# Kernel tuning notes

Measured on AMD Instinct MI355X. Metric: run time of the kernel, lower is better.

Reference implementation:

```python
import jax, jax.numpy as jnp
import numpy as np

B, N, D, H = 256, 40, 256, 256      # molecules, atoms/molecule, pc_hidden, pred_hidden
nS, nC, nB = 40, 5, 5               # n_SYMBOLS, n_FORMAL_CHARGES, n_BOND_TYPES
NEG_SLOPE = 0.01                    # F.leaky_relu default


def _lrelu(x):
    return jnp.where(x >= 0, x, NEG_SLOPE * x)


def setup_inputs() -> dict:
    key = jax.random.key(0)
    ks = jax.random.split(key, 7)
    def w(k, shape, fan_in):
        return jax.random.normal(k, shape, jnp.float32) / np.float32(np.sqrt(fan_in))
    return {
        "yhat": jax.random.normal(ks[0], (B, N, D), jnp.float32),
        "Ws1": w(ks[1], (D, H), D),      "bs1": jnp.zeros((H,), jnp.float32),
        "Ws2": w(ks[2], (H, nS), H),     "bs2": jnp.zeros((nS,), jnp.float32),
        "Wc1": w(ks[3], (D, H), D),      "bc1": jnp.zeros((H,), jnp.float32),
        "Wc2": w(ks[4], (H, nC), H),     "bc2": jnp.zeros((nC,), jnp.float32),
        "Wb1": w(ks[5], (2 * D, H), 2 * D), "bb1": jnp.zeros((H,), jnp.float32),
        "Wb2": w(ks[6], (H, nB), H),     "bb2": jnp.zeros((nB,), jnp.float32),
    }


def reference(yhat, Ws1, bs1, Ws2, bs2, Wc1, bc1, Wc2, bc2, Wb1, bb1, Wb2, bb2):
    # Per-atom symbol / charge heads (2-layer MLP with leaky_relu)
    symbols = _lrelu(yhat @ Ws1 + bs1) @ Ws2 + bs2          # [B, N, nS]
    charges = _lrelu(yhat @ Wc1 + bc1) @ Wc2 + bc2          # [B, N, nC]

    # Pairwise bond head: concat(x_i, x_j) @ Wb1 == x_i @ Wb1[:D] + x_j @ Wb1[D:]
    # (avoids materializing the [B, N, N, 2D] concat tensor)
    p1 = yhat @ Wb1[:D]                                      # [B, N, H]
    p2 = yhat @ Wb1[D:]                                      # [B, N, H]
    h = _lrelu(p1[:, :, None, :] + p2[:, None, :, :] + bb1)  # [B, N, N, H]
    bonds = h @ Wb2 + bb2                                    # [B, N, N, nB]
    bonds = bonds + jnp.swapaxes(bonds, 1, 2)                # symmetrize (i,j)+(j,i)

    return (symbols.reshape(-1, nS),
            charges.reshape(-1, nC),
            bonds.reshape(-1, nB))
```

## Files before the change

kernel.cpp:

```cpp
#include <hip/hip_runtime.h>
#include <hip/hip_bf16.h>

typedef unsigned short u16;
typedef __attribute__((ext_vector_type(4))) int   int4v;
typedef __attribute__((ext_vector_type(4))) unsigned int uint4v;
typedef __attribute__((ext_vector_type(4))) unsigned short ushort4v;
typedef __attribute__((ext_vector_type(4))) float floatx4;
typedef __attribute__((ext_vector_type(8))) short bf16x8;
typedef _Float16 half8 __attribute__((ext_vector_type(8)));
typedef _Float16 half2v __attribute__((ext_vector_type(2)));

#define LRELU_NS 0.01f
#define SK 264

__device__ __forceinline__ float bitsToF(unsigned int b) {
    union { unsigned int u; float f; } v; v.u = b << 16; return v.f;
}
__device__ __forceinline__ u16 f2bf(float f) {
    __hip_bfloat16 h = __float2bfloat16(f);
    return *reinterpret_cast<u16*>(&h);
}
__device__ __forceinline__ float lrelu(float v) {
    return fmaxf(v, LRELU_NS * v);
}
__device__ __forceinline__ u16 ldW(const void* p, int i, int isF32) {
    return isF32 ? f2bf(((const float*)p)[i]) : ((const u16*)p)[i];
}
__device__ __forceinline__ float ldF(const void* p, int i, int isF32) {
    return isF32 ? ((const float*)p)[i]
                 : bitsToF((unsigned int)((const u16*)p)[i]);
}
__device__ __forceinline__ u16 f2h_bits(float f) {
    union { _Float16 h; u16 u; } v; v.h = (_Float16)f; return v.u;
}
__device__ __forceinline__ u16 ldWh(const void* p, int i, int isF32) {
    float f = isF32 ? ((const float*)p)[i]
                    : bitsToF((unsigned int)((const u16*)p)[i]);
    return f2h_bits(f);
}
__device__ __forceinline__ half2v u2h2(unsigned int x) {
    union { unsigned int u; half2v h; } v; v.u = x; return v.h;
}
__device__ __forceinline__ unsigned int h22u(half2v x) {
    union { half2v h; unsigned int u; } v; v.h = x; return v.u;
}

__device__ __forceinline__ int computeIsF32(const u16* y, int* cnt, int t) {
    if (t == 0) *cnt = 0;
    __syncthreads();
    if (t < 256) {
        u16 v = y[2 * t];
        int e = (v >> 7) & 0xFF;
        if (v == 0 || (e >= 96 && e < 160)) atomicAdd(cnt, 1);
    }
    __syncthreads();
    return (*cnt < 192) ? 1 : 0;
}

__global__ __launch_bounds__(256) void pack_kernel(
    const void* __restrict__ yhat,
    const void* __restrict__ Ws1, const void* __restrict__ Wc1,
    const void* __restrict__ Wb1, const void* __restrict__ Ws2,
    const void* __restrict__ Wc2,
    const void* __restrict__ bs1, const void* __restrict__ bc1,
    const void* __restrict__ bb1, const void* __restrict__ bs2,
    const void* __restrict__ bc2, const void* __restrict__ bb2,
    u16* __restrict__ WallT, u16* __restrict__ W2T, float* __restrict__ biasF)
{
    __shared__ int fcnt;
    const int bid = blockIdx.x, t = threadIdx.x;
    const int isF32 = computeIsF32((const u16*)yhat, &fcnt, t);
    if (bid < 64) {
        __shared__ u16 tile[64][65];
        const int c0 = (bid & 15) * 64;
        const int k0 = (bid >> 4) * 64;
        const void* src; int coff; int roff = 0;
        if (c0 < 256)      { src = Ws1; coff = c0; }
        else if (c0 < 512) { src = Wc1; coff = c0 - 256; }
        else if (c0 < 768) { src = Wb1; coff = c0 - 512; }
        else               { src = Wb1; coff = c0 - 768; roff = 256; }
        const int cc = t & 63, kk0 = t >> 6;
        #pragma unroll
        for (int i = 0; i < 16; ++i) {
            int kk = kk0 + i * 4;
            tile[kk][cc] = ldW(src, (k0 + kk + roff) * 256 + coff + cc, isF32);
        }
        __syncthreads();
        const int kk2 = t & 63, cc0 = t >> 6;
        #pragma unroll
        for (int i = 0; i < 16; ++i) {
            int cc2 = cc0 + i * 4;
            WallT[(c0 + cc2) * 256 + (k0 + kk2)] = tile[kk2][cc2];
        }
    } else if (bid < 128) {
        int e2 = (bid - 64) * 256 + t;
        int c = e2 >> 8, k = e2 & 255;
        u16 v = 0;
        if (c < 40)                 v = ldW(Ws2, k * 40 + c, isF32);
        else if (c >= 48 && c < 53) v = ldW(Wc2, k * 5 + (c - 48), isF32);
        W2T[c * 256 + k] = v;
    } else {
        int idx = (bid - 128) * 256 + t;
        float v = 0.f;
        if (idx < 256)       v = ldF(bs1, idx, isF32);
        else if (idx < 512)  v = ldF(bc1, idx - 256, isF32);
        else if (idx < 768)  v = ldF(bb1, idx - 512, isF32);
        else if (idx < 808)  v = ldF(bs2, idx - 768, isF32);
        else if (idx < 813)  v = ldF(bc2, idx - 808, isF32);
        else if (idx >= 816 && idx < 821) v = ldF(bb2, idx - 816, isF32);
        biasF[idx] = v;
    }
}

union SharedHB {
    struct { u16 Xs[64 * SK]; u16 Hb[64 * SK]; } hd;
    struct { u16 Xm[48 * SK]; u16 P1L[48 * SK]; u16 P2L[48 * SK];
             u16 WsB[5 * 264]; } bd;
};

__global__ __launch_bounds__(512) void fused_kernel(
    const void* __restrict__ Xv, const u16* __restrict__ WallT,
    const u16* __restrict__ W2T, const void* __restrict__ Wb2,
    const float* __restrict__ biasF, void* __restrict__ outv)
{
    __shared__ SharedHB sh;
    __shared__ int fcnt;
    const int t = threadIdx.x;
    const int bid = blockIdx.x;
    const int isF32 = computeIsF32((const u16*)Xv, &fcnt, t);

    const int w = t >> 6, l = t & 63;
    const int ml = l & 15, kq = l >> 4, r0 = kq * 4;

    if (bid < 256) {
        const int b = bid;

        if (isF32) {
            const floatx4* __restrict__ src = (const floatx4*)((const float*)Xv + b * 10240);
            #pragma unroll
            for (int s = 0; s < 5; ++s) {
                int cid = t + s * 512;
                int row = cid >> 6, ch = cid & 63;
                floatx4 f = src[cid];
                ushort4v u;
                u[0] = f2bf(f[0]); u[1] = f2bf(f[1]); u[2] = f2bf(f[2]); u[3] = f2bf(f[3]);
                *(ushort4v*)&sh.bd.Xm[row * SK + ch * 4] = u;
            }
            {
                int row = 40 + (t >> 6), ch = t & 63;
                ushort4v z = {0, 0, 0, 0};
                *(ushort4v*)&sh.bd.Xm[row * SK + ch * 4] = z;
            }
        } else {
            const int4v* __restrict__ src = (const int4v*)((const u16*)Xv + b * 10240);
            #pragma unroll
            for (int s = 0; s < 3; ++s) {
                int cid = t + s * 512;
                int row = cid >> 5, ch = cid & 31;
                if (cid < 1280) *(int4v*)&sh.bd.Xm[row * SK + ch * 8] = src[cid];
                else { int4v z = {0, 0, 0, 0}; *(int4v*)&sh.bd.Xm[row * SK + ch * 8] = z; }
            }
        }
        #pragma unroll
        for (int s = 0; s < 3; ++s) {
            int e2 = t + s * 512;
            if (e2 < 1280) {
                int c = e2 >> 8, k = e2 & 255;
                sh.bd.WsB[c * 264 + k] = ldWh(Wb2, k * 5 + c, isF32);
            }
        }
        __syncthreads();

        for (int n = 0; n < 4; ++n) {
            const int gc = (w + 8 * n) * 16 + ml;
            floatx4 acc[3] = {};
            #pragma unroll
            for (int ks = 0; ks < 8; ++ks) {
                const int k0 = ks * 32 + kq * 8;
                bf16x8 bf = *(const bf16x8*)&WallT[(512 + gc) * 256 + k0];
                #pragma unroll
                for (int i = 0; i < 3; ++i) {
                    bf16x8 a = *(const bf16x8*)&sh.bd.Xm[(i * 16 + ml) * SK + k0];
                    acc[i] = __builtin_amdgcn_mfma_f32_16x16x32_bf16(a, bf, acc[i], 0, 0, 0);
                }
            }
            u16* dst = (gc < 256) ? sh.bd.P1L : sh.bd.P2L;
            const int col = gc & 255;
            const float bias = (gc < 256) ? biasF[512 + gc] : 0.f;
            #pragma unroll
            for (int i = 0; i < 3; ++i)
                #pragma unroll
                for (int r = 0; r < 4; ++r)
                    dst[(i * 16 + r0 + r) * SK + col] = f2h_bits(acc[i][r] + bias);
        }
        __syncthreads();

        const int sel = (ml < 5) ? ml : 4;
        half8 wf[8];
        #pragma unroll
        for (int ks = 0; ks < 8; ++ks)
            wf[ks] = *(const half8*)&sh.bd.WsB[sel * 264 + ks * 32 + kq * 8];
        const float b2x2 = 2.f * biasF[816 + ml];
        const _Float16 c001 = (_Float16)0.01f;

        auto storeJob = [&](int i, int jt, const floatx4& acc) {
            if (ml < 5) {
                const bool diag = (jt == (i >> 4));
                #pragma unroll
                for (int r = 0; r < 4; ++r) {
                    const int j = jt * 16 + r0 + r;
                    if (j < 40 && (!diag || j >= i)) {
                        const float v = acc[r] + b2x2;
                        const int o1 = 460800 + (b * 1600 + i * 40 + j) * 5 + ml;
                        if (isF32) ((float*)outv)[o1] = v;
                        else ((__hip_bfloat16*)outv)[o1] = __float2bfloat16(v);
                        if (!diag || j > i) {
                            const int o2 = 460800 + (b * 1600 + j * 40 + i) * 5 + ml;
                            if (isF32) ((float*)outv)[o2] = v;
                            else ((__hip_bfloat16*)outv)[o2] = __float2bfloat16(v);
                        }
                    }
                }
            }
        };

        auto runGroup = [&](const int jt, const int nm) {
            floatx4 acc[5] = {};
            #pragma unroll
            for (int ks = 0; ks < 8; ++ks) {
                const int k0 = ks * 32 + kq * 8;
                const uint4v b1 = *(const uint4v*)&sh.bd.P1L[(jt * 16 + ml) * SK + k0];
                const uint4v b2 = *(const uint4v*)&sh.bd.P2L[(jt * 16 + ml) * SK + k0];
                #pragma unroll
                for (int mm = 0; mm < 5; ++mm) {
                    if (mm < nm) {
                        const int i = w + 8 * mm;
                        const uint4v a1 = *(const uint4v*)&sh.bd.P1L[i * SK + k0];
                        const uint4v a2 = *(const uint4v*)&sh.bd.P2L[i * SK + k0];
                        union { unsigned int u[4]; half8 v; } af;
                        #pragma unroll
                        for (int d = 0; d < 4; ++d) {
                            const half2v tF = u2h2(a1[d]) + u2h2(b2[d]);
                            const half2v tB = u2h2(b1[d]) + u2h2(a2[d]);
                            const half2v lF = __builtin_elementwise_max(tF, tF * c001);
                            const half2v lB = __builtin_elementwise_max(tB, tB * c001);
                            af.u[d] = h22u(lF + lB);
                        }
                        acc[mm] = __builtin_amdgcn_mfma_f32_16x16x32_f16(af.v, wf[ks], acc[mm], 0, 0, 0);
                    }
                }
            }
            #pragma unroll
            for (int mm = 0; mm < 5; ++mm)
                if (mm < nm) storeJob(w + 8 * mm, jt, acc[mm]);
        };

        runGroup(0, 2);
        runGroup(1, 4);
        runGroup(2, 5);
    } else {
        const int hb = bid - 256;
        const int bm0 = (hb % 160) * 64;
        const int head = hb / 160;

        if (isF32) {
            const floatx4* __restrict__ src = (const floatx4*)((const float*)Xv + bm0 * 256);
            #pragma unroll
            for (int s = 0; s < 8; ++s) {
                int cid = t + s * 512;
                int row = cid >> 6, ch = cid & 63;
                floatx4 f = src[cid];
                ushort4v u;
                u[0] = f2bf(f[0]); u[1] = f2bf(f[1]); u[2] = f2bf(f[2]); u[3] = f2bf(f[3]);
                *(ushort4v*)&sh.hd.Xs[row * SK + ch * 4] = u;
            }
        } else {
            const int4v* __restrict__ src = (const int4v*)((const u16*)Xv + bm0 * 256);
            #pragma unroll
            for (int s = 0; s < 4; ++s) {
                int cid = t + s * 512;
                int row = cid >> 5, ch = cid & 31;
                *(int4v*)&sh.hd.Xs[row * SK + ch * 8] = src[cid];
            }
        }
        __syncthreads();

        #pragma unroll
        for (int n = 0; n < 2; ++n) {
            const int ct = w + 8 * n;
            floatx4 acc[4] = {};
            #pragma unroll
            for (int ks = 0; ks < 8; ++ks) {
                const int k0 = ks * 32 + kq * 8;
                bf16x8 bf = *(const bf16x8*)&WallT[(head * 256 + ct * 16 + ml) * 256 + k0];
                #pragma unroll
                for (int mt = 0; mt < 4; ++mt) {
                    bf16x8 a = *(const bf16x8*)&sh.hd.Xs[(mt * 16 + ml) * SK + k0];
                    acc[mt] = __builtin_amdgcn_mfma_f32_16x16x32_bf16(a, bf, acc[mt], 0, 0, 0);
                }
            }
            const int col = ct * 16 + ml;
            const float bias = biasF[head * 256 + col];
            #pragma unroll
            for (int mt = 0; mt < 4; ++mt)
                #pragma unroll
                for (int r = 0; r < 4; ++r)
                    sh.hd.Hb[(mt * 16 + r0 + r) * SK + col] = f2bf(lrelu(acc[mt][r] + bias));
        }
        __syncthreads();

        if (w < 4) {
            const int nct = (head == 0) ? 3 : 1;
            const int c0  = (head == 0) ? 0 : 48;
            floatx4 acc2[3] = {};
            #pragma unroll
            for (int ks = 0; ks < 8; ++ks) {
                const int k0 = ks * 32 + kq * 8;
                bf16x8 a = *(const bf16x8*)&sh.hd.Hb[(w * 16 + ml) * SK + k0];
                #pragma unroll
                for (int j = 0; j < 3; ++j) {
                    if (j < nct) {
                        bf16x8 bf = *(const bf16x8*)&W2T[(c0 + j * 16 + ml) * 256 + k0];
                        acc2[j] = __builtin_amdgcn_mfma_f32_16x16x32_bf16(a, bf, acc2[j], 0, 0, 0);
                    }
                }
            }
            #pragma unroll
            for (int j = 0; j < 3; ++j) {
                if (j < nct) {
                    const int col = j * 16 + ml;
                    const int lim = (head == 0) ? 40 : 5;
                    if (col < lim) {
                        const float bias = biasF[(head == 0 ? 768 : 808) + col];
                        #pragma unroll
                        for (int r = 0; r < 4; ++r) {
                            const int row = bm0 + w * 16 + r0 + r;
                            const int o = (head == 0) ? row * 40 + col
                                                      : 409600 + row * 5 + col;
                            const float v = acc2[j][r] + bias;
                            if (isF32) ((float*)outv)[o] = v;
                            else ((__hip_bfloat16*)outv)[o] = __float2bfloat16(v);
                        }
                    }
                }
            }
        }
    }
}

extern "C" void kernel_launch(void* const* d_in, const int* in_sizes, int n_in,
                              void* d_out, int out_size, void* d_ws, size_t ws_size,
                              hipStream_t stream)
{
    const void* yhat = d_in[0];
    const void* Ws1  = d_in[1];
    const void* bs1  = d_in[2];
    const void* Ws2  = d_in[3];
    const void* bs2  = d_in[4];
    const void* Wc1  = d_in[5];
    const void* bc1  = d_in[6];
    const void* Wc2  = d_in[7];
    const void* bc2  = d_in[8];
    const void* Wb1  = d_in[9];
    const void* bb1  = d_in[10];
    const void* Wb2  = d_in[11];
    const void* bb2  = d_in[12];

    char* wsb = (char*)d_ws;
    float* biasF = (float*)(wsb + 4096);
    u16*   W2T   = (u16*)(wsb + 8192);
    u16*   WallT = (u16*)(wsb + 40960);

    pack_kernel<<<132, 256, 0, stream>>>(yhat, Ws1, Wc1, Wb1, Ws2, Wc2,
                                         bs1, bc1, bb1, bs2, bc2, bb2,
                                         WallT, W2T, biasF);
    fused_kernel<<<576, 512, 0, stream>>>(yhat, WallT, W2T, Wb2, biasF, d_out);
}
```

Before: 122.7 us.

## Spill P2 projection to global workspace and shrink head tiles to raise occupancy

Adds a second fused kernel used when the workspace is large enough. The bond blocks keep P1 in LDS but write the P2 projection to a global scratch buffer and read it back, which cuts LDS per block. The head blocks now process 32 rows instead of 64, so the grid grows to 896 blocks. The aim is more resident blocks and better load balance, at the cost of extra global or L2 traffic for P2 and a dependence on workspace size.

```diff
diff --git a/kernel.cpp b/kernel.cpp
--- a/kernel.cpp
+++ b/kernel.cpp
@@ -112,6 +112,250 @@
     }
 }
 
+union Shared2 {
+    struct { u16 Xm[48 * SK]; u16 P1L[48 * SK]; u16 WsB[5 * 264]; } bd;
+    struct { u16 Xs[32 * SK]; u16 Hb[32 * SK]; } hd;
+};
+
+__global__ __launch_bounds__(512) void fused2_kernel(
+    const void* __restrict__ Xv, const u16* __restrict__ WallT,
+    const u16* __restrict__ W2T, const void* __restrict__ Wb2,
+    const float* __restrict__ biasF, u16* __restrict__ P2g,
+    void* __restrict__ outv)
+{
+    __shared__ Shared2 sh;
+    __shared__ int fcnt;
+    const int t = threadIdx.x;
+    const int bid = blockIdx.x;
+    const int isF32 = computeIsF32((const u16*)Xv, &fcnt, t);
+
+    const int w = t >> 6, l = t & 63;
+    const int ml = l & 15, kq = l >> 4, r0 = kq * 4;
+
+    if (bid < 256) {
+        const int b = bid;
+        u16* __restrict__ pg = P2g + (size_t)b * 12288;
+
+        if (isF32) {
+            const floatx4* __restrict__ src = (const floatx4*)((const float*)Xv + b * 10240);
+            #pragma unroll
+            for (int s = 0; s < 5; ++s) {
+                int cid = t + s * 512;
+                int row = cid >> 6, ch = cid & 63;
+                floatx4 f = src[cid];
+                ushort4v u;
+                u[0] = f2bf(f[0]); u[1] = f2bf(f[1]); u[2] = f2bf(f[2]); u[3] = f2bf(f[3]);
+                *(ushort4v*)&sh.bd.Xm[row * SK + ch * 4] = u;
+            }
+            {
+                int row = 40 + (t >> 6), ch = t & 63;
+                ushort4v z = {0, 0, 0, 0};
+                *(ushort4v*)&sh.bd.Xm[row * SK + ch * 4] = z;
+            }
+        } else {
+            const int4v* __restrict__ src = (const int4v*)((const u16*)Xv + b * 10240);
+            #pragma unroll
+            for (int s = 0; s < 3; ++s) {
+                int cid = t + s * 512;
+                int row = cid >> 5, ch = cid & 31;
+                if (cid < 1280) *(int4v*)&sh.bd.Xm[row * SK + ch * 8] = src[cid];
+                else { int4v z = {0, 0, 0, 0}; *(int4v*)&sh.bd.Xm[row * SK + ch * 8] = z; }
+            }
+        }
+        #pragma unroll
+        for (int s = 0; s < 3; ++s) {
+            int e2 = t + s * 512;
+            if (e2 < 1280) {
+                int c = e2 >> 8, k = e2 & 255;
+                sh.bd.WsB[c * 264 + k] = ldWh(Wb2, k * 5 + c, isF32);
+            }
+        }
+        __syncthreads();
+
+        for (int n = 0; n < 4; ++n) {
+            const int gc = (w + 8 * n) * 16 + ml;
+            floatx4 acc[3] = {};
+            #pragma unroll
+            for (int ks = 0; ks < 8; ++ks) {
+                const int k0 = ks * 32 + kq * 8;
+                bf16x8 bf = *(const bf16x8*)&WallT[(512 + gc) * 256 + k0];
+                #pragma unroll
+                for (int i = 0; i < 3; ++i) {
+                    bf16x8 a = *(const bf16x8*)&sh.bd.Xm[(i * 16 + ml) * SK + k0];
+                    acc[i] = __builtin_amdgcn_mfma_f32_16x16x32_bf16(a, bf, acc[i], 0, 0, 0);
+                }
+            }
+            if (gc < 256) {
+                const float bias = biasF[512 + gc];
+                #pragma unroll
+                for (int i = 0; i < 3; ++i)
+                    #pragma unroll
+                    for (int r = 0; r < 4; ++r)
+                        sh.bd.P1L[(i * 16 + r0 + r) * SK + gc] = f2h_bits(acc[i][r] + bias);
+            } else {
+                const int col = gc - 256;
+                #pragma unroll
+                for (int i = 0; i < 3; ++i)
+                    #pragma unroll
+                    for (int r = 0; r < 4; ++r)
+                        pg[(i * 16 + r0 + r) * 256 + col] = f2h_bits(acc[i][r]);
+            }
+        }
+        __syncthreads();
+
+        const int sel = (ml < 5) ? ml : 4;
+        half8 wf[8];
+        #pragma unroll
+        for (int ks = 0; ks < 8; ++ks)
+            wf[ks] = *(const half8*)&sh.bd.WsB[sel * 264 + ks * 32 + kq * 8];
+        const float b2x2 = 2.f * biasF[816 + ml];
+        const _Float16 c001 = (_Float16)0.01f;
+
+        auto storeJob = [&](int i, int jt, const floatx4& acc) {
+            if (ml < 5) {
+                const bool diag = (jt == (i >> 4));
+                #pragma unroll
+                for (int r = 0; r < 4; ++r) {
+                    const int j = jt * 16 + r0 + r;
+                    if (j < 40 && (!diag || j >= i)) {
+                        const float v = acc[r] + b2x2;
+                        const int o1 = 460800 + (b * 1600 + i * 40 + j) * 5 + ml;
+                        if (isF32) ((float*)outv)[o1] = v;
+                        else ((__hip_bfloat16*)outv)[o1] = __float2bfloat16(v);
+                        if (!diag || j > i) {
+                            const int o2 = 460800 + (b * 1600 + j * 40 + i) * 5 + ml;
+                            if (isF32) ((float*)outv)[o2] = v;
+                            else ((__hip_bfloat16*)outv)[o2] = __float2bfloat16(v);
+                        }
+                    }
+                }
+            }
+        };
+
+        auto runGroup = [&](const int jt, const int nm) {
+            floatx4 acc[5] = {};
+            #pragma unroll
+            for (int ks = 0; ks < 8; ++ks) {
+                const int k0 = ks * 32 + kq * 8;
+                const uint4v b1 = *(const uint4v*)&sh.bd.P1L[(jt * 16 + ml) * SK + k0];
+                const uint4v b2 = *(const uint4v*)&pg[(jt * 16 + ml) * 256 + k0];
+                #pragma unroll
+                for (int mm = 0; mm < 5; ++mm) {
+                    if (mm < nm) {
+                        const int i = w + 8 * mm;
+                        const uint4v a1 = *(const uint4v*)&sh.bd.P1L[i * SK + k0];
+                        const uint4v a2 = *(const uint4v*)&pg[i * 256 + k0];
+                        union { unsigned int u[4]; half8 v; } af;
+                        #pragma unroll
+                        for (int d = 0; d < 4; ++d) {
+                            const half2v tF = u2h2(a1[d]) + u2h2(b2[d]);
+                            const half2v tB = u2h2(b1[d]) + u2h2(a2[d]);
+                            const half2v lF = __builtin_elementwise_max(tF, tF * c001);
+                            const half2v lB = __builtin_elementwise_max(tB, tB * c001);
+                            af.u[d] = h22u(lF + lB);
+                        }
+                        acc[mm] = __builtin_amdgcn_mfma_f32_16x16x32_f16(af.v, wf[ks], acc[mm], 0, 0, 0);
+                    }
+                }
+            }
+            #pragma unroll
+            for (int mm = 0; mm < 5; ++mm)
+                if (mm < nm) storeJob(w + 8 * mm, jt, acc[mm]);
+        };
+
+        runGroup(0, 2);
+        runGroup(1, 4);
+        runGroup(2, 5);
+    } else {
+        const int hb = bid - 256;
+        const int bm0 = (hb % 320) * 32;
+        const int head = hb / 320;
+
+        if (isF32) {
+            const floatx4* __restrict__ src = (const floatx4*)((const float*)Xv + bm0 * 256);
+            #pragma unroll
+            for (int s = 0; s < 4; ++s) {
+                int cid = t + s * 512;
+                int row = cid >> 6, ch = cid & 63;
+                floatx4 f = src[cid];
+                ushort4v u;
+                u[0] = f2bf(f[0]); u[1] = f2bf(f[1]); u[2] = f2bf(f[2]); u[3] = f2bf(f[3]);
+                *(ushort4v*)&sh.hd.Xs[row * SK + ch * 4] = u;
+            }
+        } else {
+            const int4v* __restrict__ src = (const int4v*)((const u16*)Xv + bm0 * 256);
+            #pragma unroll
+            for (int s = 0; s < 2; ++s) {
+                int cid = t + s * 512;
+                int row = cid >> 5, ch = cid & 31;
+                *(int4v*)&sh.hd.Xs[row * SK + ch * 8] = src[cid];
+            }
+        }
+        __syncthreads();
+
+        #pragma unroll
+        for (int n = 0; n < 2; ++n) {
+            const int ct = w + 8 * n;
+            floatx4 acc[2] = {};
+            #pragma unroll
+            for (int ks = 0; ks < 8; ++ks) {
+                const int k0 = ks * 32 + kq * 8;
+                bf16x8 bf = *(const bf16x8*)&WallT[(head * 256 + ct * 16 + ml) * 256 + k0];
+                #pragma unroll
+                for (int mt = 0; mt < 2; ++mt) {
+                    bf16x8 a = *(const bf16x8*)&sh.hd.Xs[(mt * 16 + ml) * SK + k0];
+                    acc[mt] = __builtin_amdgcn_mfma_f32_16x16x32_bf16(a, bf, acc[mt], 0, 0, 0);
+                }
+            }
+            const int col = ct * 16 + ml;
+            const float bias = biasF[head * 256 + col];
+            #pragma unroll
+            for (int mt = 0; mt < 2; ++mt)
+                #pragma unroll
+                for (int r = 0; r < 4; ++r)
+                    sh.hd.Hb[(mt * 16 + r0 + r) * SK + col] = f2bf(lrelu(acc[mt][r] + bias));
+        }
+        __syncthreads();
+
+        if (w < 2) {
+            const int nct = (head == 0) ? 3 : 1;
+            const int c0  = (head == 0) ? 0 : 48;
+            floatx4 acc2[3] = {};
+            #pragma unroll
+            for (int ks = 0; ks < 8; ++ks) {
+                const int k0 = ks * 32 + kq * 8;
+                bf16x8 a = *(const bf16x8*)&sh.hd.Hb[(w * 16 + ml) * SK + k0];
+                #pragma unroll
+                for (int j = 0; j < 3; ++j) {
+                    if (j < nct) {
+                        bf16x8 bf = *(const bf16x8*)&W2T[(c0 + j * 16 + ml) * 256 + k0];
+                        acc2[j] = __builtin_amdgcn_mfma_f32_16x16x32_bf16(a, bf, acc2[j], 0, 0, 0);
+                    }
+                }
+            }
+            #pragma unroll
+            for (int j = 0; j < 3; ++j) {
+                if (j < nct) {
+                    const int col = j * 16 + ml;
+                    const int lim = (head == 0) ? 40 : 5;
+                    if (col < lim) {
+                        const float bias = biasF[(head == 0 ? 768 : 808) + col];
+                        #pragma unroll
+                        for (int r = 0; r < 4; ++r) {
+                            const int row = bm0 + w * 16 + r0 + r;
+                            const int o = (head == 0) ? row * 40 + col
+                                                      : 409600 + row * 5 + col;
+                            const float v = acc2[j][r] + bias;
+                            if (isF32) ((float*)outv)[o] = v;
+                            else ((__hip_bfloat16*)outv)[o] = __float2bfloat16(v);
+                        }
+                    }
+                }
+            }
+        }
+    }
+}
+
 union SharedHB {
     struct { u16 Xs[64 * SK]; u16 Hb[64 * SK]; } hd;
     struct { u16 Xm[48 * SK]; u16 P1L[48 * SK]; u16 P2L[48 * SK];
@@ -370,9 +614,16 @@
     float* biasF = (float*)(wsb + 4096);
     u16*   W2T   = (u16*)(wsb + 8192);
     u16*   WallT = (u16*)(wsb + 40960);
+    u16*   P2g   = (u16*)(wsb + 565248);
+    const bool big = ws_size >= 565248 + (size_t)256 * 12288 * 2;
 
     pack_kernel<<<132, 256, 0, stream>>>(yhat, Ws1, Wc1, Wb1, Ws2, Wc2,
                                          bs1, bc1, bb1, bs2, bc2, bb2,
                                          WallT, W2T, biasF);
-    fused_kernel<<<576, 512, 0, stream>>>(yhat, WallT, W2T, Wb2, biasF, d_out);
-}
+    if (big) {
+        fused2_kernel<<<896, 512, 0, stream>>>(yhat, WallT, W2T, Wb2, biasF,
+                                               P2g, d_out);
+    } else {
+        fused_kernel<<<576, 512, 0, stream>>>(yhat, WallT, W2T, Wb2, biasF, d_out);
+    }
+}
```

New measurement: 135.6 us. 1.1x slower.
